# Performance work log

Hardware: AMD Instinct MI355X
Metric: run time of the kernel (lower is better)

## Reference

```python
import math
import jax, jax.numpy as jnp
import numpy as np

DIM = 4096
N_HEADS = 32
N_KV_HEADS = 8
HEAD_DIM = DIM // N_HEADS          # 128
N_REP = N_HEADS // N_KV_HEADS      # 4
BATCH = 2
SEQLEN = 2048
MAX_BATCH = 2
MAX_SEQ = 2048
THETA = 10000.0


def _precompute_freqs(dim, end, theta=THETA):
    freqs = 1.0 / theta ** (np.arange(0, dim, 2)[: dim // 2].astype(np.float32) / dim)
    t = np.arange(end, dtype=np.float32)
    ang = np.outer(t, freqs)  # [end, dim//2]
    return jnp.asarray(np.cos(ang), jnp.float32), jnp.asarray(np.sin(ang), jnp.float32)


def setup_inputs() -> dict:
    key = jax.random.key(0)
    ks = jax.random.split(key, 6)
    x = jax.random.normal(ks[0], (BATCH, SEQLEN, DIM), jnp.float32)
    scale = 0.02
    wq = jax.random.normal(ks[1], (DIM, N_HEADS * HEAD_DIM), jnp.float32) * scale
    wk = jax.random.normal(ks[2], (DIM, N_KV_HEADS * HEAD_DIM), jnp.float32) * scale
    wv = jax.random.normal(ks[3], (DIM, N_KV_HEADS * HEAD_DIM), jnp.float32) * scale
    wo = jax.random.normal(ks[4], (N_HEADS * HEAD_DIM, DIM), jnp.float32) * scale
    cache_k = jnp.zeros((MAX_BATCH, MAX_SEQ, N_KV_HEADS, HEAD_DIM), jnp.float32)
    cache_v = jnp.zeros((MAX_BATCH, MAX_SEQ, N_KV_HEADS, HEAD_DIM), jnp.float32)
    freqs_cos, freqs_sin = _precompute_freqs(HEAD_DIM, SEQLEN)
    # additive causal mask, [S, S]
    mask = jnp.where(jnp.tril(jnp.ones((SEQLEN, SEQLEN), bool)), 0.0, -1e9).astype(jnp.float32)
    return {"x": x, "wq": wq, "wk": wk, "wv": wv, "wo": wo,
            "cache_k": cache_k, "cache_v": cache_v,
            "freqs_cos": freqs_cos, "freqs_sin": freqs_sin,
            "mask": mask, "start_pos": 0}


def _apply_rotary(t, cos, sin):
    # t: [B, S, H, D]; cos/sin: [S, D/2] -> broadcast [1, S, 1, D/2]
    B, S, H, D = t.shape
    tr = t.reshape(B, S, H, D // 2, 2)
    re, im = tr[..., 0], tr[..., 1]
    c = cos[None, :, None, :]
    s = sin[None, :, None, :]
    out = jnp.stack([re * c - im * s, re * s + im * c], axis=-1)
    return out.reshape(B, S, H, D)


def reference(x, wq, wk, wv, wo, cache_k, cache_v, freqs_cos, freqs_sin, mask, start_pos):
    B, S, D = x.shape
    xq = (x @ wq).reshape(B, S, N_HEADS, HEAD_DIM)
    xk = (x @ wk).reshape(B, S, N_KV_HEADS, HEAD_DIM)
    xv = (x @ wv).reshape(B, S, N_KV_HEADS, HEAD_DIM)
    xq = _apply_rotary(xq, freqs_cos, freqs_sin)
    xk = _apply_rotary(xk, freqs_cos, freqs_sin)
    # KV-cache write (start_pos is a static Python int)
    ck = cache_k.at[:B, start_pos:start_pos + S].set(xk)
    cv = cache_v.at[:B, start_pos:start_pos + S].set(xv)
    keys = ck[:B, :start_pos + S]    # [B, T, KVH, D]
    values = cv[:B, :start_pos + S]
    # GQA: repeat kv heads
    keys = jnp.repeat(keys, N_REP, axis=2)      # [B, T, H, D]
    values = jnp.repeat(values, N_REP, axis=2)
    scores = jnp.einsum('bqhd,bkhd->bhqk', xq, keys) / math.sqrt(HEAD_DIM)
    scores = scores + mask[None, None, :, :]
    probs = jax.nn.softmax(scores.astype(jnp.float32), axis=-1).astype(xq.dtype)
    out = jnp.einsum('bhqk,bkhd->bqhd', probs, values).reshape(B, S, N_HEADS * HEAD_DIM)
    return out @ wo
```

## Files before the change

### kernel.cpp

```cpp
#include <hip/hip_runtime.h>
#include <stdint.h>

typedef __attribute__((ext_vector_type(4))) float f32x4;
typedef __attribute__((ext_vector_type(4))) unsigned short u16x4;
typedef __attribute__((ext_vector_type(8))) unsigned short u16x8;
typedef __attribute__((ext_vector_type(8))) short s16x8;

#define NH   32
#define NKV  8
#define HD   128
#define SEQ  2048
#define MTOK 4096

__device__ __forceinline__ float b2f(unsigned short u) {
  union { float f; unsigned int i; } v; v.i = ((unsigned int)u) << 16; return v.f;
}
__device__ __forceinline__ unsigned short f2b(float f) {
  unsigned int i = __float_as_uint(f);
  return (unsigned short)((i + 0x7fffu + ((i >> 16) & 1u)) >> 16);
}

__global__ void convert_f32_bf16(const float* __restrict__ in,
                                 unsigned short* __restrict__ out, int n4) {
  int i = blockIdx.x * 256 + threadIdx.x;
  if (i >= n4) return;
  f32x4 v = *(const f32x4*)(in + (size_t)i * 4);
  u16x4 r;
  r.x = f2b(v.x); r.y = f2b(v.y); r.z = f2b(v.z); r.w = f2b(v.w);
  *(u16x4*)(out + (size_t)i * 4) = r;
}

__global__ void tconv(const float* __restrict__ W, unsigned short* __restrict__ WT, int N) {
  __shared__ float tile[32][33];
  int k0 = blockIdx.x * 32, n0 = blockIdx.y * 32;
  int t = threadIdx.x;
  int r = t >> 3;
  int c = (t & 7) * 4;
  f32x4 v = *(const f32x4*)&W[(size_t)(k0 + r) * N + n0 + c];
  tile[r][c + 0] = v.x; tile[r][c + 1] = v.y; tile[r][c + 2] = v.z; tile[r][c + 3] = v.w;
  __syncthreads();
  u16x4 o;
  o.x = f2b(tile[c + 0][r]); o.y = f2b(tile[c + 1][r]);
  o.z = f2b(tile[c + 2][r]); o.w = f2b(tile[c + 3][r]);
  *(u16x4*)&WT[(size_t)(n0 + r) * 4096 + k0 + c] = o;
}

__global__ void vtrans(const unsigned short* __restrict__ vb, unsigned short* __restrict__ vtb) {
  __shared__ unsigned short tile[32][36];
  int s0 = blockIdx.x * 32, d0 = blockIdx.y * 32;
  int bkv = blockIdx.z; int b = bkv >> 3, kvh = bkv & 7;
  int t = threadIdx.x;
  int r = t >> 3, c = (t & 7) * 4;
  u16x4 v = *(const u16x4*)&vb[((size_t)(b * SEQ + s0 + r) * NKV + kvh) * HD + d0 + c];
  tile[r][c + 0] = v.x; tile[r][c + 1] = v.y; tile[r][c + 2] = v.z; tile[r][c + 3] = v.w;
  __syncthreads();
  u16x4 o;
  o.x = tile[c + 0][r]; o.y = tile[c + 1][r]; o.z = tile[c + 2][r]; o.w = tile[c + 3][r];
  *(u16x4*)&vtb[((size_t)(b * NKV + kvh) * HD + d0 + r) * SEQ + s0 + c] = o;
}

__global__ void rope_k(unsigned short* __restrict__ x, const float* __restrict__ cs,
                       const float* __restrict__ sn, int nhShift, int total) {
  int i = blockIdx.x * 256 + threadIdx.x;
  if (i >= total) return;
  int g = i & 15;
  int rem = i >> 4;
  int h = rem & ((1 << nhShift) - 1);
  int sb = rem >> nhShift;
  int s = sb & (SEQ - 1);
  size_t base = (((size_t)sb << nhShift) + h) * HD + g * 8;
  u16x8 v = *(u16x8*)(x + base);
  f32x4 c = *(const f32x4*)(cs + s * 64 + g * 4);
  f32x4 sv = *(const f32x4*)(sn + s * 64 + g * 4);
#pragma unroll
  for (int j = 0; j < 4; ++j) {
    float re = b2f(v[2 * j]), im = b2f(v[2 * j + 1]);
    float cj = c[j], sj = sv[j];
    v[2 * j]     = f2b(re * cj - im * sj);
    v[2 * j + 1] = f2b(re * sj + im * cj);
  }
  *(u16x8*)(x + base) = v;
}

template <typename OutT>
__global__ __launch_bounds__(256, 2)
void gemm_bt(const unsigned short* __restrict__ A, const unsigned short* __restrict__ BT,
             OutT* __restrict__ C, int M, int N, int K) {
  __shared__ __align__(16) unsigned short As[128 * 64];
  __shared__ __align__(16) unsigned short Bs[128 * 64];
  const int t = threadIdx.x;
  const int lane = t & 63;
  const int w = t >> 6;
  const int l15 = lane & 15, l4 = lane >> 4;
  const int wm = w >> 1, wn = w & 1;
  const int m0 = blockIdx.x * 128, n0 = blockIdx.y * 128;

  f32x4 acc[4][4];
#pragma unroll
  for (int i = 0; i < 4; ++i)
#pragma unroll
    for (int j = 0; j < 4; ++j) acc[i][j] = (f32x4)(0.0f);

  for (int k0 = 0; k0 < K; k0 += 64) {
#pragma unroll
    for (int p = 0; p < 4; ++p) {
      int cb = p * 256 + w * 64;
      int c = cb + lane;
      int row = c >> 3, co = (c & 7) * 8;
      const unsigned short* srcA = A + (size_t)(m0 + row) * K + k0 + co;
      const unsigned short* srcB = BT + (size_t)(n0 + row) * K + k0 + co;
      __builtin_amdgcn_global_load_lds((const __attribute__((address_space(1))) void*)srcA,
                                       (__attribute__((address_space(3))) void*)(As + cb * 8),
                                       16, 0, 0);
      __builtin_amdgcn_global_load_lds((const __attribute__((address_space(1))) void*)srcB,
                                       (__attribute__((address_space(3))) void*)(Bs + cb * 8),
                                       16, 0, 0);
    }
    __syncthreads();
    s16x8 af[4][2], bfr[4][2];
#pragma unroll
    for (int mi = 0; mi < 4; ++mi)
#pragma unroll
      for (int kk = 0; kk < 2; ++kk)
        af[mi][kk] = *(const s16x8*)&As[(wm * 64 + mi * 16 + l15) * 64 + kk * 32 + l4 * 8];
#pragma unroll
    for (int ni = 0; ni < 4; ++ni)
#pragma unroll
      for (int kk = 0; kk < 2; ++kk)
        bfr[ni][kk] = *(const s16x8*)&Bs[(wn * 64 + ni * 16 + l15) * 64 + kk * 32 + l4 * 8];
#pragma unroll
    for (int kk = 0; kk < 2; ++kk)
#pragma unroll
      for (int mi = 0; mi < 4; ++mi)
#pragma unroll
        for (int ni = 0; ni < 4; ++ni)
          acc[mi][ni] = __builtin_amdgcn_mfma_f32_16x16x32_bf16(af[mi][kk], bfr[ni][kk],
                                                                acc[mi][ni], 0, 0, 0);
    __syncthreads();
  }
#pragma unroll
  for (int mi = 0; mi < 4; ++mi)
#pragma unroll
    for (int ni = 0; ni < 4; ++ni) {
      int col = n0 + wn * 64 + ni * 16 + l15;
#pragma unroll
      for (int r = 0; r < 4; ++r) {
        int row = m0 + wm * 64 + mi * 16 + l4 * 4 + r;
        if constexpr (sizeof(OutT) == 2)
          C[(size_t)row * N + col] = f2b(acc[mi][ni][r]);
        else
          C[(size_t)row * N + col] = acc[mi][ni][r];
      }
    }
}

__global__ __launch_bounds__(256, 2)
void attn_kernel(const unsigned short* __restrict__ qb, const unsigned short* __restrict__ kb,
                 const unsigned short* __restrict__ vtb, unsigned short* __restrict__ ab) {
  __shared__ __align__(16) unsigned short Ks[64 * 136];
  __shared__ __align__(16) unsigned short Vs[128 * 72];
  __shared__ __align__(16) unsigned short Ps[4 * 16 * 72];
  const int bx = (int)blockIdx.x;
  const int qt = 31 - (bx >> 6);
  const int hb = bx & 63;
  const int h = hb >> 1;
  const int b = hb & 1;
  const int kvh = h >> 2;
  const int t = threadIdx.x, lane = t & 63, w = t >> 6;
  const int l15 = lane & 15, l4 = lane >> 4;
  const int q0 = qt * 64;
  const float SCALE = 0.08838834764831845f;

  size_t qoff = ((size_t)(b * SEQ + q0 + w * 16 + l15) * NH + h) * HD;
  s16x8 qf[4];
#pragma unroll
  for (int kk = 0; kk < 4; ++kk) qf[kk] = *(const s16x8*)(qb + qoff + kk * 32 + l4 * 8);

  f32x4 accO[8];
#pragma unroll
  for (int n = 0; n < 8; ++n) accO[n] = (f32x4)(0.0f);
  float mrow[4] = {-1e30f, -1e30f, -1e30f, -1e30f};
  float lrow[4] = {0.f, 0.f, 0.f, 0.f};
  unsigned short* Pw = Ps + w * 16 * 72;

  u16x8 kreg[4], vreg[4];
  auto load_tile = [&](int k0) {
#pragma unroll
    for (int p = 0; p < 4; ++p) {
      int c = p * 256 + t;
      int krow = c >> 4, kco = (c & 15) * 8;
      kreg[p] = *(const u16x8*)(kb + ((size_t)(b * SEQ + k0 + krow) * NKV + kvh) * HD + kco);
      int vrow = c >> 3, vco = (c & 7) * 8;
      vreg[p] = *(const u16x8*)(vtb + ((size_t)(b * NKV + kvh) * HD + vrow) * SEQ + k0 + vco);
    }
  };
  auto write_tile = [&]() {
#pragma unroll
    for (int p = 0; p < 4; ++p) {
      int c = p * 256 + t;
      *(u16x8*)&Ks[(c >> 4) * 136 + (c & 15) * 8] = kreg[p];
      *(u16x8*)&Vs[(c >> 3) * 72 + (c & 7) * 8] = vreg[p];
    }
  };

  load_tile(0);
  write_tile();
  __syncthreads();

  for (int kt = 0; kt <= qt; ++kt) {
    f32x4 sc[4];
#pragma unroll
    for (int g = 0; g < 4; ++g) sc[g] = (f32x4)(0.0f);
    __builtin_amdgcn_s_setprio(1);
#pragma unroll
    for (int g = 0; g < 4; ++g)
#pragma unroll
      for (int kk = 0; kk < 4; ++kk) {
        s16x8 kf = *(const s16x8*)&Ks[(g * 16 + l15) * 136 + kk * 32 + l4 * 8];
        sc[g] = __builtin_amdgcn_mfma_f32_16x16x32_bf16(qf[kk], kf, sc[g], 0, 0, 0);
      }
    __builtin_amdgcn_s_setprio(0);

    if (kt < qt) load_tile((kt + 1) * 64);

    if (kt == qt) {
#pragma unroll
      for (int g = 0; g < 4; ++g)
#pragma unroll
        for (int r = 0; r < 4; ++r) {
          int key = g * 16 + l15;
          int qr = w * 16 + l4 * 4 + r;
          float v = sc[g][r] * SCALE;
          sc[g][r] = (key <= qr) ? v : -1e30f;
        }
    } else {
#pragma unroll
      for (int g = 0; g < 4; ++g)
#pragma unroll
        for (int r = 0; r < 4; ++r) sc[g][r] *= SCALE;
    }
    float resc[4], newm[4];
#pragma unroll
    for (int r = 0; r < 4; ++r) {
      float tm = fmaxf(fmaxf(sc[0][r], sc[1][r]), fmaxf(sc[2][r], sc[3][r]));
      tm = fmaxf(tm, __shfl_xor(tm, 1));
      tm = fmaxf(tm, __shfl_xor(tm, 2));
      tm = fmaxf(tm, __shfl_xor(tm, 4));
      tm = fmaxf(tm, __shfl_xor(tm, 8));
      newm[r] = fmaxf(mrow[r], tm);
      resc[r] = __expf(mrow[r] - newm[r]);
      mrow[r] = newm[r];
    }
    float pv[4][4];
#pragma unroll
    for (int g = 0; g < 4; ++g)
#pragma unroll
      for (int r = 0; r < 4; ++r) pv[g][r] = __expf(sc[g][r] - newm[r]);
#pragma unroll
    for (int r = 0; r < 4; ++r) {
      float s = pv[0][r] + pv[1][r] + pv[2][r] + pv[3][r];
      s += __shfl_xor(s, 1);
      s += __shfl_xor(s, 2);
      s += __shfl_xor(s, 4);
      s += __shfl_xor(s, 8);
      lrow[r] = lrow[r] * resc[r] + s;
    }
#pragma unroll
    for (int g = 0; g < 4; ++g)
#pragma unroll
      for (int r = 0; r < 4; ++r) Pw[(l4 * 4 + r) * 72 + g * 16 + l15] = f2b(pv[g][r]);
#pragma unroll
    for (int n = 0; n < 8; ++n)
#pragma unroll
      for (int r = 0; r < 4; ++r) accO[n][r] *= resc[r];
    s16x8 pf[2];
    pf[0] = *(const s16x8*)&Pw[l15 * 72 + l4 * 8];
    pf[1] = *(const s16x8*)&Pw[l15 * 72 + 32 + l4 * 8];
    __builtin_amdgcn_s_setprio(1);
#pragma unroll
    for (int n = 0; n < 8; ++n)
#pragma unroll
      for (int kk = 0; kk < 2; ++kk) {
        s16x8 vf = *(const s16x8*)&Vs[(n * 16 + l15) * 72 + kk * 32 + l4 * 8];
        accO[n] = __builtin_amdgcn_mfma_f32_16x16x32_bf16(pf[kk], vf, accO[n], 0, 0, 0);
      }
    __builtin_amdgcn_s_setprio(0);

    __syncthreads();
    if (kt < qt) {
      write_tile();
      __syncthreads();
    }
  }
  float inv[4];
#pragma unroll
  for (int r = 0; r < 4; ++r) inv[r] = 1.0f / lrow[r];
#pragma unroll
  for (int n = 0; n < 8; ++n)
#pragma unroll
    for (int r = 0; r < 4; ++r) {
      int s = q0 + w * 16 + l4 * 4 + r;
      ab[((size_t)(b * SEQ + s) * NH + h) * HD + n * 16 + l15] = f2b(accO[n][r] * inv[r]);
    }
}

extern "C" void kernel_launch(void* const* d_in, const int* in_sizes, int n_in,
                              void* d_out, int out_size, void* d_ws, size_t ws_size,
                              hipStream_t stream) {
  const float* x = (const float*)d_in[0];
  const float* wq = (const float*)d_in[1];
  const float* wk = (const float*)d_in[2];
  const float* wv = (const float*)d_in[3];
  const float* wo = (const float*)d_in[4];
  const float* fcos = (const float*)d_in[7];
  const float* fsin = (const float*)d_in[8];
  float* out = (float*)d_out;

  unsigned short* ws = (unsigned short*)d_ws;
  unsigned short* xb  = ws;
  unsigned short* wqT = ws + 16777216;
  unsigned short* wkT = ws + 33554432;
  unsigned short* wvT = ws + 37748736;
  unsigned short* woT = ws + 41943040;
  unsigned short* qb  = ws + 58720256;
  unsigned short* kb  = ws + 75497472;
  unsigned short* vb  = ws + 79691776;
  unsigned short* vtb = ws + 83886080;
  unsigned short* ab  = ws + 88080384;

  convert_f32_bf16<<<(4194304 + 255) / 256, 256, 0, stream>>>(x, xb, 4194304);
  tconv<<<dim3(128, 128), 256, 0, stream>>>(wq, wqT, 4096);
  tconv<<<dim3(128, 32), 256, 0, stream>>>(wk, wkT, 1024);
  tconv<<<dim3(128, 32), 256, 0, stream>>>(wv, wvT, 1024);
  tconv<<<dim3(128, 128), 256, 0, stream>>>(wo, woT, 4096);

  gemm_bt<unsigned short><<<dim3(32, 32), 256, 0, stream>>>(xb, wqT, qb, MTOK, 4096, 4096);
  gemm_bt<unsigned short><<<dim3(32, 8), 256, 0, stream>>>(xb, wkT, kb, MTOK, 1024, 4096);
  gemm_bt<unsigned short><<<dim3(32, 8), 256, 0, stream>>>(xb, wvT, vb, MTOK, 1024, 4096);

  rope_k<<<(2097152 + 255) / 256, 256, 0, stream>>>(qb, fcos, fsin, 5, 2097152);
  rope_k<<<(524288 + 255) / 256, 256, 0, stream>>>(kb, fcos, fsin, 3, 524288);

  vtrans<<<dim3(64, 4, 16), 256, 0, stream>>>(vb, vtb);

  attn_kernel<<<2048, 256, 0, stream>>>(qb, kb, vtb, ab);

  gemm_bt<float><<<dim3(32, 32), 256, 0, stream>>>(ab, woT, out, MTOK, 4096, 4096);
}
```

Measured before the change: 1.031 ms.

## Add 256x256-tile double-buffered GEMM with direct global-to-LDS loads for Q and O projections

Adds a new GEMM kernel that uses 256x256 output tiles with 512 threads and double-buffered LDS stages. The stages are filled through global_load_lds with an XOR swizzle, and MFMA issue priority is raised while the math runs. The kernel replaces the 128x128 gemm_bt for the two large 4096x4096x4096 projections. The aim is more data reuse per tile and overlap of loads with MFMA work. In exchange it uses more registers and LDS (64KB per block), and the grid shrinks to 256 blocks, which may leave part of the machine underused.

```diff
diff --git a/kernel.cpp b/kernel.cpp
--- a/kernel.cpp
+++ b/kernel.cpp
@@ -150,6 +150,101 @@
           C[(size_t)row * N + col] = f2b(acc[mi][ni][r]);
         else
           C[(size_t)row * N + col] = acc[mi][ni][r];
+      }
+    }
+}
+
+template <typename OutT>
+__global__ __launch_bounds__(512, 2)
+void gemm256(const unsigned short* __restrict__ A, const unsigned short* __restrict__ BT,
+             OutT* __restrict__ C, int M, int N, int K) {
+  __shared__ __align__(16) unsigned short As[2][256 * 64];
+  __shared__ __align__(16) unsigned short Bs[2][256 * 64];
+  const int t = threadIdx.x;
+  const int lane = t & 63, w = t >> 6;
+  const int l15 = lane & 15, l4 = lane >> 4;
+  const int wr = w >> 2, wc = w & 3;
+  const int m0 = blockIdx.x * 256, n0 = blockIdx.y * 256;
+  const int xk = l15 & 7;
+
+  f32x4 acc[8][4];
+#pragma unroll
+  for (int i = 0; i < 8; ++i)
+#pragma unroll
+    for (int j = 0; j < 4; ++j) acc[i][j] = (f32x4)(0.0f);
+
+  auto stage = [&](int buf, int k0) {
+#pragma unroll
+    for (int p = 0; p < 4; ++p) {
+      int e = p * 4096 + t * 8;
+      int r = e >> 6;
+      int bb = (e >> 3) & 7;
+      int sc = (bb ^ (r & 7)) << 3;
+      int cb = p * 4096 + w * 512;
+      __builtin_amdgcn_global_load_lds(
+          (const __attribute__((address_space(1))) void*)(A + (size_t)(m0 + r) * K + k0 + sc),
+          (__attribute__((address_space(3))) void*)(&As[buf][cb]), 16, 0, 0);
+      __builtin_amdgcn_global_load_lds(
+          (const __attribute__((address_space(1))) void*)(BT + (size_t)(n0 + r) * K + k0 + sc),
+          (__attribute__((address_space(3))) void*)(&Bs[buf][cb]), 16, 0, 0);
+    }
+  };
+
+  const int NT = K >> 6;
+  stage(0, 0);
+  asm volatile("s_waitcnt vmcnt(0)" ::: "memory");
+  __builtin_amdgcn_s_barrier();
+  __builtin_amdgcn_sched_barrier(0);
+
+  for (int kt = 0; kt < NT; ++kt) {
+    const int buf = kt & 1;
+    if (kt + 1 < NT) {
+      stage(buf ^ 1, (kt + 1) * 64);
+      asm volatile("s_waitcnt vmcnt(8)" ::: "memory");
+    } else {
+      asm volatile("s_waitcnt vmcnt(0)" ::: "memory");
+    }
+    __builtin_amdgcn_s_barrier();
+    __builtin_amdgcn_sched_barrier(0);
+
+#pragma unroll
+    for (int kk = 0; kk < 2; ++kk) {
+      s16x8 af[8], bfr[4];
+#pragma unroll
+      for (int mi = 0; mi < 8; ++mi) {
+        int R = wr * 128 + mi * 16 + l15;
+        af[mi] = *(const s16x8*)&As[buf][R * 64 + (((kk * 4 + l4) ^ xk) << 3)];
+      }
+#pragma unroll
+      for (int ni = 0; ni < 4; ++ni) {
+        int R = wc * 64 + ni * 16 + l15;
+        bfr[ni] = *(const s16x8*)&Bs[buf][R * 64 + (((kk * 4 + l4) ^ xk) << 3)];
+      }
+      __builtin_amdgcn_s_setprio(1);
+#pragma unroll
+      for (int mi = 0; mi < 8; ++mi)
+#pragma unroll
+        for (int ni = 0; ni < 4; ++ni)
+          acc[mi][ni] = __builtin_amdgcn_mfma_f32_16x16x32_bf16(af[mi], bfr[ni],
+                                                                acc[mi][ni], 0, 0, 0);
+      __builtin_amdgcn_s_setprio(0);
+    }
+    __builtin_amdgcn_s_barrier();
+    __builtin_amdgcn_sched_barrier(0);
+  }
+
+#pragma unroll
+  for (int mi = 0; mi < 8; ++mi)
+#pragma unroll
+    for (int ni = 0; ni < 4; ++ni) {
+      int col = n0 + wc * 64 + ni * 16 + l15;
+      int rowb = m0 + wr * 128 + mi * 16 + l4 * 4;
+#pragma unroll
+      for (int r = 0; r < 4; ++r) {
+        if constexpr (sizeof(OutT) == 2)
+          C[(size_t)(rowb + r) * N + col] = f2b(acc[mi][ni][r]);
+        else
+          C[(size_t)(rowb + r) * N + col] = acc[mi][ni][r];
       }
     }
 }
@@ -334,7 +429,7 @@
   tconv<<<dim3(128, 32), 256, 0, stream>>>(wv, wvT, 1024);
   tconv<<<dim3(128, 128), 256, 0, stream>>>(wo, woT, 4096);
 
-  gemm_bt<unsigned short><<<dim3(32, 32), 256, 0, stream>>>(xb, wqT, qb, MTOK, 4096, 4096);
+  gemm256<unsigned short><<<dim3(16, 16), 512, 0, stream>>>(xb, wqT, qb, MTOK, 4096, 4096);
   gemm_bt<unsigned short><<<dim3(32, 8), 256, 0, stream>>>(xb, wkT, kb, MTOK, 1024, 4096);
   gemm_bt<unsigned short><<<dim3(32, 8), 256, 0, stream>>>(xb, wvT, vb, MTOK, 1024, 4096);
 
@@ -345,5 +440,5 @@
 
   attn_kernel<<<2048, 256, 0, stream>>>(qb, kb, vtb, ab);
 
-  gemm_bt<float><<<dim3(32, 32), 256, 0, stream>>>(ab, woT, out, MTOK, 4096, 4096);
-}
+  gemm256<float><<<dim3(16, 16), 512, 0, stream>>>(ab, woT, out, MTOK, 4096, 4096);
+}
```

After: 932.8 us. -9.5%, faster.
